# Performance work log

Measured on AMD Instinct MI355X. Metric: run time of the kernel, lower is better.

Reference implementation:

```python
import jax, jax.numpy as jnp
import numpy as np

B, S, C, H, RANK = 8, 1024, 1280, 8, 4
MERGE_SCALE = 1.0   # self.scale
LORA_SCALE = 1.0    # scale arg passed to __call__ (defaults 1.0)


def setup_inputs() -> dict:
    key = jax.random.key(0)
    ks = jax.random.split(key, 20)
    std = 1.0 / np.sqrt(C)
    rstd = 1.0 / np.sqrt(RANK)
    d = {
        "hidden_states": jax.random.normal(ks[0], (B, S, C), jnp.float32),
        "pose_feature": jax.random.normal(ks[1], (B, S, C), jnp.float32),
        # qkv_merge Linear (init to zeros in the module; use small random to exercise the path)
        "qkv_merge_w": jax.random.normal(ks[2], (C, C), jnp.float32) * (0.02 * std),
        "qkv_merge_b": jax.random.normal(ks[3], (C,), jnp.float32) * 0.01,
        # attn.to_q/k/v (bias-free, diffusers default) and to_out[0] (with bias). Stored [in, out].
        "wq": jax.random.normal(ks[4], (C, C), jnp.float32) * std,
        "wk": jax.random.normal(ks[5], (C, C), jnp.float32) * std,
        "wv": jax.random.normal(ks[6], (C, C), jnp.float32) * std,
        "wo": jax.random.normal(ks[7], (C, C), jnp.float32) * std,
        "bo": jax.random.normal(ks[8], (C,), jnp.float32) * 0.01,
        # LoRA layers: down [in, rank], up [rank, out] (up is zeros at init; random here)
        "q_lora_down": jax.random.normal(ks[9], (C, RANK), jnp.float32) * std,
        "q_lora_up": jax.random.normal(ks[10], (RANK, C), jnp.float32) * rstd,
        "k_lora_down": jax.random.normal(ks[11], (C, RANK), jnp.float32) * std,
        "k_lora_up": jax.random.normal(ks[12], (RANK, C), jnp.float32) * rstd,
        "v_lora_down": jax.random.normal(ks[13], (C, RANK), jnp.float32) * std,
        "v_lora_up": jax.random.normal(ks[14], (RANK, C), jnp.float32) * rstd,
        "out_lora_down": jax.random.normal(ks[15], (C, RANK), jnp.float32) * std,
        "out_lora_up": jax.random.normal(ks[16], (RANK, C), jnp.float32) * rstd,
        "num_heads": H,
    }
    return d


def _lora(x, down, up):
    # LoRALinearLayer with network_alpha=None -> scale factor 1
    return (x @ down) @ up


def reference(hidden_states, pose_feature, qkv_merge_w, qkv_merge_b,
              wq, wk, wv, wo, bo,
              q_lora_down, q_lora_up, k_lora_down, k_lora_up,
              v_lora_down, v_lora_up, out_lora_down, out_lora_up,
              num_heads):
    b, s, c = hidden_states.shape
    dh = c // num_heads
    # gated pose-merge (query_condition and key_value_condition -> shared qkv source)
    merged = (hidden_states + pose_feature) @ qkv_merge_w + qkv_merge_b
    x = merged * MERGE_SCALE + hidden_states  # [b, s, c]
    # LoRA-augmented projections
    q = x @ wq + LORA_SCALE * _lora(x, q_lora_down, q_lora_up)
    k = x @ wk + LORA_SCALE * _lora(x, k_lora_down, k_lora_up)
    v = x @ wv + LORA_SCALE * _lora(x, v_lora_down, v_lora_up)
    # head_to_batch_dim -> [b, h, s, dh]
    q = q.reshape(b, s, num_heads, dh).transpose(0, 2, 1, 3)
    k = k.reshape(b, s, num_heads, dh).transpose(0, 2, 1, 3)
    v = v.reshape(b, s, num_heads, dh).transpose(0, 2, 1, 3)
    # attn.get_attention_scores: baddbmm scaled by head_dim**-0.5, then softmax
    scores = jnp.einsum('bhqd,bhkd->bhqk', q, k) * (dh ** -0.5)
    probs = jax.nn.softmax(scores, axis=-1)
    out = jnp.einsum('bhqk,bhkd->bhqd', probs, v)
    # batch_to_head_dim -> [b, s, c]
    out = out.transpose(0, 2, 1, 3).reshape(b, s, c)
    # output projection + LoRA; to_out[1] is dropout (identity at eval)
    out = out @ wo + bo + LORA_SCALE * _lora(out, out_lora_down, out_lora_up)
    # residual_connection=False, rescale_output_factor=1.0
    return out
```

## Files before the change

### kernel.cpp

```cpp
#include <hip/hip_runtime.h>
#include <stdint.h>

typedef unsigned short u16;
typedef __attribute__((ext_vector_type(8))) short short8;
typedef __attribute__((ext_vector_type(4))) float f32x4;

__device__ __forceinline__ float b2f(u16 x){
  union { unsigned u; float f; } v; v.u = ((unsigned)x) << 16; return v.f;
}
__device__ __forceinline__ float b2fs(short x){ return b2f((u16)x); }
__device__ __forceinline__ u16 f2b(float f){
  union { float f; unsigned u; } v; v.f = f;
  unsigned u = v.u;
  u += 0x7FFFu + ((u >> 16) & 1u);
  return (u16)(u >> 16);
}
__device__ __forceinline__ float ldg_f(const void* p, int i, int f32){
  return f32 ? ((const float*)p)[i] : b2f(((const u16*)p)[i]);
}
__device__ __forceinline__ void gld16(const void* g, void* l){
  __builtin_amdgcn_global_load_lds(
      (__attribute__((address_space(1))) void*)(g),
      (__attribute__((address_space(3))) void*)(l), 16, 0, 0);
}
__device__ __forceinline__ unsigned lds_addr(const void* p){
  return (unsigned)(size_t)(__attribute__((address_space(3))) const void*)p;
}
__device__ __forceinline__ short8 ds_r128(unsigned addr){
  short8 r;
  asm volatile("ds_read_b128 %0, %1" : "=v"(r) : "v"(addr));
  return r;
}

__global__ void detect_dtype(const u16* __restrict__ hid, int* __restrict__ flag){
  if (blockIdx.x == 0){
    int lane = threadIdx.x & 63;
    int plaus = 0;
    for (int i = lane; i < 512; i += 64){
      u16 v = hid[2 * i];
      int e = (v >> 7) & 0xFF;
      if ((e >= 100 && e <= 140) || (v & 0x7FFF) == 0) plaus++;
    }
    #pragma unroll
    for (int xm = 1; xm < 64; xm <<= 1) plaus += __shfl_xor(plaus, xm, 64);
    if (threadIdx.x == 0) *flag = (plaus < 400) ? 1 : 0;
  }
}

__global__ void make_t(const void* __restrict__ hid, const void* __restrict__ pose,
                       u16* __restrict__ t, const int* __restrict__ flag){
  int base = (blockIdx.x * 256 + threadIdx.x) * 8;
  short8 o;
  if (*flag){
    #pragma unroll
    for (int j = 0; j < 2; j++){
      float4 a = *(const float4*)((const float*)hid  + base + j * 4);
      float4 b = *(const float4*)((const float*)pose + base + j * 4);
      o[j * 4 + 0] = (short)f2b(a.x + b.x);
      o[j * 4 + 1] = (short)f2b(a.y + b.y);
      o[j * 4 + 2] = (short)f2b(a.z + b.z);
      o[j * 4 + 3] = (short)f2b(a.w + b.w);
    }
  } else {
    short8 a = *(const short8*)((const u16*)hid  + base);
    short8 b = *(const short8*)((const u16*)pose + base);
    #pragma unroll
    for (int j = 0; j < 8; j++) o[j] = (short)f2b(b2fs(a[j]) + b2fs(b[j]));
  }
  *(short8*)(t + base) = o;
}

__global__ void prep_w(const void* __restrict__ w, const void* __restrict__ dn,
                       const void* __restrict__ up, u16* __restrict__ WT,
                       int rowOff, float sc, const int* __restrict__ flag)
{
  __shared__ float tile[64][65];
  const int f = *flag;
  const int k0 = blockIdx.x * 64, n0 = blockIdx.y * 64;
  const int tr  = threadIdx.x >> 2;
  const int tc0 = (threadIdx.x & 3) * 16;
  #pragma unroll
  for (int i = 0; i < 16; i++)
    tile[tr][tc0 + i] = ldg_f(w, (k0 + tr) * 1280 + n0 + tc0 + i, f);
  __syncthreads();
  const int n = n0 + tr;
  float upv[4];
  if (dn){
    #pragma unroll
    for (int r = 0; r < 4; r++) upv[r] = ldg_f(up, r * 1280 + n, f);
  }
  u16 tmp[16];
  #pragma unroll
  for (int i = 0; i < 16; i++){
    int k = k0 + tc0 + i;
    float val = tile[tc0 + i][tr];
    if (dn){
      #pragma unroll
      for (int r = 0; r < 4; r++)
        val += ldg_f(dn, k * 4 + r, f) * upv[r];
    }
    tmp[i] = f2b(val * sc);
  }
  u16* dst = &WT[(rowOff + n) * 1280 + k0 + tc0];
  #pragma unroll
  for (int i = 0; i < 4; i++)
    *(ushort4*)(dst + i * 4) = *(ushort4*)(tmp + i * 4);
}

template<bool BIAS, bool RESID, bool RAWOUT>
__global__ __launch_bounds__(256) void gemm_bt(
    const u16* __restrict__ A, const u16* __restrict__ BT,
    const void* __restrict__ bias, const void* __restrict__ resid,
    void* __restrict__ Cout, int NOUT, int Kdim, const int* __restrict__ flag)
{
  __shared__ alignas(16) u16 As[128 * 32];
  __shared__ alignas(16) u16 Bs[128 * 32];
  const int tid  = threadIdx.x;
  const int lane = tid & 63;
  const int w    = tid >> 6;
  const int wm   = w >> 1, wn = w & 1;
  const int quad = lane >> 4, l15 = lane & 15;
  const int tileM = blockIdx.y << 7;
  const int tileN = blockIdx.x << 7;
  const int f32 = (BIAS || RESID || RAWOUT) ? *flag : 0;

  f32x4 acc[4][4];
  #pragma unroll
  for (int mi = 0; mi < 4; mi++)
    #pragma unroll
    for (int ni = 0; ni < 4; ni++)
      acc[mi][ni] = (f32x4){0.f, 0.f, 0.f, 0.f};

  for (int k0 = 0; k0 < Kdim; k0 += 32){
    {
      int c = tid;
      gld16(&A [(tileM + (c >> 2)) * Kdim + k0 + ((c & 3) << 3)], (char*)As + c * 16);
      gld16(&BT[(tileN + (c >> 2)) * Kdim + k0 + ((c & 3) << 3)], (char*)Bs + c * 16);
      c = tid + 256;
      gld16(&A [(tileM + (c >> 2)) * Kdim + k0 + ((c & 3) << 3)], (char*)As + c * 16);
      gld16(&BT[(tileN + (c >> 2)) * Kdim + k0 + ((c & 3) << 3)], (char*)Bs + c * 16);
    }
    __syncthreads();

    short8 af[4], bfr[4];
    #pragma unroll
    for (int mi = 0; mi < 4; mi++)
      af[mi] = *(const short8*)(As + (wm * 64 + mi * 16 + l15) * 32 + quad * 8);
    #pragma unroll
    for (int ni = 0; ni < 4; ni++)
      bfr[ni] = *(const short8*)(Bs + (wn * 64 + ni * 16 + l15) * 32 + quad * 8);
    #pragma unroll
    for (int mi = 0; mi < 4; mi++)
      #pragma unroll
      for (int ni = 0; ni < 4; ni++)
        acc[mi][ni] = __builtin_amdgcn_mfma_f32_16x16x32_bf16(
            af[mi], bfr[ni], acc[mi][ni], 0, 0, 0);
    __syncthreads();
  }

  #pragma unroll
  for (int mi = 0; mi < 4; mi++){
    #pragma unroll
    for (int ni = 0; ni < 4; ni++){
      int col = tileN + wn * 64 + ni * 16 + l15;
      float bv = 0.f;
      if (BIAS) bv = ldg_f(bias, col, f32);
      #pragma unroll
      for (int r = 0; r < 4; r++){
        int row = tileM + wm * 64 + mi * 16 + quad * 4 + r;
        float v = acc[mi][ni][r] + bv;
        if (RESID) v += ldg_f(resid, row * NOUT + col, f32);
        if (RAWOUT && f32) ((float*)Cout)[row * NOUT + col] = v;
        else               ((u16*)Cout)[row * NOUT + col]   = f2b(v);
      }
    }
  }
}

#define GPHASE(KK, MH)                                                         \
  {                                                                            \
    if ((MH) == 0){                                                            \
      _Pragma("unroll")                                                        \
      for (int n = 0; n < 4; n++){                                             \
        int R = wn * 64 + n * 16 + l15;                                        \
        int sl = (KK) * 4 + quad;                                              \
        bfr[n] = ds_r128(lds_addr(&Bsm[b][R * 64 + ((sl ^ (R & 7)) << 3)]));   \
      }                                                                        \
    }                                                                          \
    short8 af[4];                                                              \
    _Pragma("unroll")                                                          \
    for (int j = 0; j < 4; j++){                                               \
      int R = wm * 128 + ((MH) * 4 + j) * 16 + l15;                            \
      int sl = (KK) * 4 + quad;                                                \
      af[j] = ds_r128(lds_addr(&Asm[b][R * 64 + ((sl ^ (R & 7)) << 3)]));      \
    }                                                                          \
    __builtin_amdgcn_s_barrier();                                              \
    asm volatile("s_waitcnt lgkmcnt(0)" ::: "memory");                         \
    __builtin_amdgcn_sched_barrier(0);                                         \
    __builtin_amdgcn_s_setprio(1);                                             \
    _Pragma("unroll")                                                          \
    for (int j = 0; j < 4; j++)                                                \
      _Pragma("unroll")                                                        \
      for (int n = 0; n < 4; n++)                                              \
        acc[(MH) * 4 + j][n] = __builtin_amdgcn_mfma_f32_16x16x32_bf16(        \
            af[j], bfr[n], acc[(MH) * 4 + j][n], 0, 0, 0);                     \
    __builtin_amdgcn_s_setprio(0);                                             \
    __builtin_amdgcn_s_barrier();                                              \
  }

__global__ __launch_bounds__(512, 2) void gemm256_qkv(
    const u16* __restrict__ A, const u16* __restrict__ BT,
    u16* __restrict__ Cout, u16* __restrict__ vtg,
    int gridX, int Kdim)
{
  __shared__ alignas(16) u16 Asm[2][256 * 64];
  __shared__ alignas(16) u16 Bsm[2][256 * 64];
  const int tid  = threadIdx.x;
  const int lane = tid & 63;
  const int w    = tid >> 6;
  const int wm   = w >> 2, wn = w & 3;
  const int quad = lane >> 4, l15 = lane & 15;

  const int nwg = gridDim.x;
  const int id  = blockIdx.x;
  const int swz = (id & 7) * (nwg >> 3) + (id >> 3);
  const int bx  = swz % gridX;
  const int by  = swz / gridX;
  const int tileM = by << 8;
  const int tileN = bx << 8;

  auto stageHalf = [&](int bufi, int half, int kt){
    const int k0 = kt << 6;
    #pragma unroll
    for (int s = 0; s < 2; s++){
      int cl   = s * 512 + tid;
      int p    = ((half & 1) << 10) + cl;
      int row  = p >> 3;
      int lslt = (p & 7) ^ (row & 7);
      if (half < 2)
        gld16(&A [(tileM + row) * Kdim + k0 + lslt * 8], (char*)Asm[bufi] + p * 16);
      else
        gld16(&BT[(tileN + row) * Kdim + k0 + lslt * 8], (char*)Bsm[bufi] + p * 16);
    }
  };

  f32x4 acc[8][4];
  #pragma unroll
  for (int mi = 0; mi < 8; mi++)
    #pragma unroll
    for (int ni = 0; ni < 4; ni++)
      acc[mi][ni] = (f32x4){0.f, 0.f, 0.f, 0.f};

  const int NT = Kdim >> 6;
  stageHalf(0, 0, 0); stageHalf(0, 1, 0); stageHalf(0, 2, 0); stageHalf(0, 3, 0);
  stageHalf(1, 0, 1); stageHalf(1, 1, 1);
  asm volatile("s_waitcnt vmcnt(4)" ::: "memory");
  __builtin_amdgcn_s_barrier();

  for (int kt = 0; kt < NT; kt++){
    const int b = kt & 1;
    short8 bfr[4];
    if (kt + 1 < NT) stageHalf(b ^ 1, 2, kt + 1);
    GPHASE(0, 0)
    if (kt + 1 < NT) stageHalf(b ^ 1, 3, kt + 1);
    GPHASE(0, 1)
    GPHASE(1, 0)
    GPHASE(1, 1)
    if (kt + 2 < NT){ stageHalf(b, 0, kt + 2); stageHalf(b, 1, kt + 2); }
    if (kt + 1 < NT){
      if (kt + 2 < NT) asm volatile("s_waitcnt vmcnt(4)" ::: "memory");
      else             asm volatile("s_waitcnt vmcnt(0)" ::: "memory");
      __builtin_amdgcn_s_barrier();
    }
  }

  if (tileN >= 2560){
    #pragma unroll
    for (int mi = 0; mi < 8; mi++){
      #pragma unroll
      for (int ni = 0; ni < 4; ni++){
        int col = tileN + wn * 64 + ni * 16 + l15;
        int hd = col - 2560;
        int hh = hd / 160;
        int dd = hd - hh * 160;
        int row0 = tileM + wm * 128 + mi * 16 + quad * 4;
        int bb = row0 >> 10;
        long addr = ((long)((bb * 8 + hh) * 160 + dd) << 10) | (long)(row0 & 1023);
        ushort4 pk;
        pk.x = f2b(acc[mi][ni][0]); pk.y = f2b(acc[mi][ni][1]);
        pk.z = f2b(acc[mi][ni][2]); pk.w = f2b(acc[mi][ni][3]);
        *(ushort4*)&vtg[addr] = pk;
      }
    }
  } else {
    #pragma unroll
    for (int mi = 0; mi < 8; mi++){
      #pragma unroll
      for (int ni = 0; ni < 4; ni++){
        int col = tileN + wn * 64 + ni * 16 + l15;
        #pragma unroll
        for (int r = 0; r < 4; r++){
          int row = tileM + wm * 128 + mi * 16 + quad * 4 + r;
          Cout[row * 2560 + col] = f2b(acc[mi][ni][r]);
        }
      }
    }
  }
}

__global__ __launch_bounds__(256, 2) void attn_mfma(
    const u16* __restrict__ qk, const u16* __restrict__ vtg,
    u16* __restrict__ out)
{
  __shared__ alignas(16) u16 Ks[2 * 64 * 160];
  __shared__ alignas(16) u16 Vt[160 * 64];
  __shared__ alignas(16) u16 Ps[4 * 32 * 72];

  const int tid  = threadIdx.x, lane = tid & 63, wv = tid >> 6;
  const int quad = lane >> 4,   l15  = lane & 15;
  const int bh = ((blockIdx.y >> 3) << 3) | blockIdx.x;
  const int qt = blockIdx.y & 7;
  const int b  = bh >> 3, h = bh & 7;
  const int rowBase = (b << 10) + (qt << 7);
  const int kBase   = b << 10;

  short8 qa[2][5];
  #pragma unroll
  for (int mi = 0; mi < 2; mi++)
    #pragma unroll
    for (int kk = 0; kk < 5; kk++)
      qa[mi][kk] = *(const short8*)&qk[
          (rowBase + wv * 32 + mi * 16 + l15) * 2560 + h * 160 + kk * 32 + quad * 8];

  f32x4 o[2][10];
  #pragma unroll
  for (int mi = 0; mi < 2; mi++)
    #pragma unroll
    for (int ni = 0; ni < 10; ni++)
      o[mi][ni] = (f32x4){0.f, 0.f, 0.f, 0.f};
  float mr[2][4], lr[2][4];
  #pragma unroll
  for (int mi = 0; mi < 2; mi++)
    #pragma unroll
    for (int r = 0; r < 4; r++){ mr[mi][r] = -1e30f; lr[mi][r] = 0.f; }

  #pragma unroll
  for (int i = 0; i < 5; i++){
    int c = tid + (i << 8);
    int kr = c / 20, kc = c % 20;
    gld16(&qk[(kBase + kr) * 2560 + 1280 + h * 160 + (kc << 3)],
          (char*)Ks + c * 16);
  }
  __syncthreads();

  int buf = 0;
  for (int kt = 0; kt < 16; kt++){
    #pragma unroll
    for (int i = 0; i < 5; i++){
      int c = tid + (i << 8);
      int d = c >> 3;
      int l = (c & 7) ^ (d & 7);
      gld16(&vtg[((bh * 160 + d) << 10) + (kt << 6) + (l << 3)],
            (char*)Vt + c * 16);
    }
    if (kt < 15){
      #pragma unroll
      for (int i = 0; i < 5; i++){
        int c = tid + (i << 8);
        int kr = c / 20, kc = c % 20;
        gld16(&qk[(kBase + ((kt + 1) << 6) + kr) * 2560 + 1280 + h * 160 + (kc << 3)],
              (char*)Ks + (buf ^ 1) * 20480 + c * 16);
      }
    }
    const u16* KsR = Ks + buf * 10240;

    f32x4 s[2][4];
    #pragma unroll
    for (int mi = 0; mi < 2; mi++)
      #pragma unroll
      for (int ni = 0; ni < 4; ni++)
        s[mi][ni] = (f32x4){0.f, 0.f, 0.f, 0.f};
    __builtin_amdgcn_s_setprio(1);
    #pragma unroll
    for (int kk = 0; kk < 5; kk++){
      #pragma unroll
      for (int ni = 0; ni < 4; ni++){
        short8 bf = *(const short8*)&KsR[(ni * 16 + l15) * 160 + kk * 32 + quad * 8];
        s[0][ni] = __builtin_amdgcn_mfma_f32_16x16x32_bf16(qa[0][kk], bf, s[0][ni], 0, 0, 0);
        s[1][ni] = __builtin_amdgcn_mfma_f32_16x16x32_bf16(qa[1][kk], bf, s[1][ni], 0, 0, 0);
      }
    }
    __builtin_amdgcn_s_setprio(0);

    float al[2][4];
    #pragma unroll
    for (int mi = 0; mi < 2; mi++){
      #pragma unroll
      for (int r = 0; r < 4; r++){
        float mx = fmaxf(fmaxf(s[mi][0][r], s[mi][1][r]),
                         fmaxf(s[mi][2][r], s[mi][3][r]));
        #pragma unroll
        for (int xm = 1; xm < 16; xm <<= 1) mx = fmaxf(mx, __shfl_xor(mx, xm, 64));
        float mn = fmaxf(mr[mi][r], mx);
        float a  = __expf(mr[mi][r] - mn);
        mr[mi][r] = mn; al[mi][r] = a;
        float sum = 0.f;
        #pragma unroll
        for (int ni = 0; ni < 4; ni++){
          float p = __expf(s[mi][ni][r] - mn);
          s[mi][ni][r] = p; sum += p;
        }
        #pragma unroll
        for (int xm = 1; xm < 16; xm <<= 1) sum += __shfl_xor(sum, xm, 64);
        lr[mi][r] = lr[mi][r] * a + sum;
      }
    }
    #pragma unroll
    for (int mi = 0; mi < 2; mi++)
      #pragma unroll
      for (int ni = 0; ni < 4; ni++)
        #pragma unroll
        for (int r = 0; r < 4; r++)
          Ps[wv * 2304 + (mi * 16 + quad * 4 + r) * 72 + ni * 16 + l15] =
              f2b(s[mi][ni][r]);
    #pragma unroll
    for (int mi = 0; mi < 2; mi++)
      #pragma unroll
      for (int ni = 0; ni < 10; ni++)
        #pragma unroll
        for (int r = 0; r < 4; r++)
          o[mi][ni][r] *= al[mi][r];

    if (kt < 15) asm volatile("s_waitcnt vmcnt(5)" ::: "memory");
    else         asm volatile("s_waitcnt vmcnt(0)" ::: "memory");
    __builtin_amdgcn_s_barrier();

    __builtin_amdgcn_s_setprio(1);
    #pragma unroll
    for (int kk2 = 0; kk2 < 2; kk2++){
      short8 pa0 = *(const short8*)&Ps[wv * 2304 + l15 * 72        + kk2 * 32 + quad * 8];
      short8 pa1 = *(const short8*)&Ps[wv * 2304 + (16 + l15) * 72 + kk2 * 32 + quad * 8];
      #pragma unroll
      for (int ni = 0; ni < 10; ni++){
        short8 vf = *(const short8*)&Vt[((ni * 16 + l15) << 6) +
                                        (((((kk2 << 2) | quad)) ^ (l15 & 7)) << 3)];
        o[0][ni] = __builtin_amdgcn_mfma_f32_16x16x32_bf16(pa0, vf, o[0][ni], 0, 0, 0);
        o[1][ni] = __builtin_amdgcn_mfma_f32_16x16x32_bf16(pa1, vf, o[1][ni], 0, 0, 0);
      }
    }
    __builtin_amdgcn_s_setprio(0);

    asm volatile("s_waitcnt vmcnt(0)" ::: "memory");
    __builtin_amdgcn_s_barrier();
    buf ^= 1;
  }

  #pragma unroll
  for (int mi = 0; mi < 2; mi++){
    #pragma unroll
    for (int r = 0; r < 4; r++){
      float inv = 1.0f / lr[mi][r];
      int row = rowBase + wv * 32 + mi * 16 + quad * 4 + r;
      #pragma unroll
      for (int ni = 0; ni < 10; ni++)
        out[row * 1280 + h * 160 + ni * 16 + l15] = f2b(o[mi][ni][r] * inv);
    }
  }
}

extern "C" void kernel_launch(void* const* d_in, const int* in_sizes, int n_in,
                              void* d_out, int out_size, void* d_ws, size_t ws_size,
                              hipStream_t stream)
{
  const void* hid  = d_in[0];
  const void* pose = d_in[1];
  const void* wm   = d_in[2];
  const void* mb   = d_in[3];
  const void* wq   = d_in[4];
  const void* wk   = d_in[5];
  const void* wv   = d_in[6];
  const void* wo   = d_in[7];
  const void* bo   = d_in[8];
  const void* qd   = d_in[9];
  const void* qu   = d_in[10];
  const void* kd   = d_in[11];
  const void* ku   = d_in[12];
  const void* vd   = d_in[13];
  const void* vu   = d_in[14];
  const void* od   = d_in[15];
  const void* ou   = d_in[16];
  (void)in_sizes; (void)n_in; (void)out_size; (void)ws_size;

  u16* ws   = (u16*)d_ws;
  u16* qk   = ws;
  u16* t    = qk;
  u16* x    = qk + 20971520;
  u16* vtg  = x + 10485760;
  u16* Wbuf = vtg + 10485760;
  u16* attnout = x;
  int* flag = (int*)(Wbuf + 4915200);

  const float qscale = 0.07905694150420949f;

  detect_dtype<<<1, 64, 0, stream>>>((const u16*)hid, flag);
  make_t<<<5120, 256, 0, stream>>>(hid, pose, t, flag);
  prep_w<<<dim3(20, 20), 256, 0, stream>>>(wm, nullptr, nullptr, Wbuf, 0, 1.0f, flag);
  gemm_bt<true, true, false><<<dim3(10, 64), 256, 0, stream>>>(
      t, Wbuf, mb, hid, x, 1280, 1280, flag);
  prep_w<<<dim3(20, 20), 256, 0, stream>>>(wq, qd, qu, Wbuf, 0, qscale, flag);
  prep_w<<<dim3(20, 20), 256, 0, stream>>>(wk, kd, ku, Wbuf, 1280, 1.0f, flag);
  prep_w<<<dim3(20, 20), 256, 0, stream>>>(wv, vd, vu, Wbuf, 2560, 1.0f, flag);
  gemm256_qkv<<<480, 512, 0, stream>>>(x, Wbuf, qk, vtg, 15, 1280);
  attn_mfma<<<dim3(8, 64), 256, 0, stream>>>(qk, vtg, attnout);
  prep_w<<<dim3(20, 20), 256, 0, stream>>>(wo, od, ou, Wbuf, 0, 1.0f, flag);
  gemm_bt<true, false, true><<<dim3(10, 64), 256, 0, stream>>>(
      attnout, Wbuf, bo, nullptr, d_out, 1280, 1280, flag);
}
```

Measured before the change: 509.1 us.

## Software-pipeline LDS fragment reads with MFMA and drop per-phase barriers in QKV GEMM

Restructures the QKV GEMM inner k-loop so LDS fragment reads for the next MFMA group are issued before the current group runs, using partial lgkmcnt waits instead of a full wait. The two barriers around each of the four phases are removed, leaving one barrier per k-tile. This is meant to hide LDS latency behind MFMA work and cut synchronization stalls. It costs more live fragment registers (four A/B buffers), which may push register pressure at 512 threads with two blocks per CU. Both B-half stages are now issued at the start of the iteration.

```diff
diff --git a/kernel.cpp b/kernel.cpp
--- a/kernel.cpp
+++ b/kernel.cpp
@@ -177,36 +177,19 @@
   }
 }
 
-#define GPHASE(KK, MH)                                                         \
-  {                                                                            \
-    if ((MH) == 0){                                                            \
-      _Pragma("unroll")                                                        \
-      for (int n = 0; n < 4; n++){                                             \
-        int R = wn * 64 + n * 16 + l15;                                        \
-        int sl = (KK) * 4 + quad;                                              \
-        bfr[n] = ds_r128(lds_addr(&Bsm[b][R * 64 + ((sl ^ (R & 7)) << 3)]));   \
-      }                                                                        \
-    }                                                                          \
-    short8 af[4];                                                              \
-    _Pragma("unroll")                                                          \
-    for (int j = 0; j < 4; j++){                                               \
-      int R = wm * 128 + ((MH) * 4 + j) * 16 + l15;                            \
-      int sl = (KK) * 4 + quad;                                                \
-      af[j] = ds_r128(lds_addr(&Asm[b][R * 64 + ((sl ^ (R & 7)) << 3)]));      \
-    }                                                                          \
-    __builtin_amdgcn_s_barrier();                                              \
-    asm volatile("s_waitcnt lgkmcnt(0)" ::: "memory");                         \
-    __builtin_amdgcn_sched_barrier(0);                                         \
-    __builtin_amdgcn_s_setprio(1);                                             \
-    _Pragma("unroll")                                                          \
-    for (int j = 0; j < 4; j++)                                                \
-      _Pragma("unroll")                                                        \
-      for (int n = 0; n < 4; n++)                                              \
-        acc[(MH) * 4 + j][n] = __builtin_amdgcn_mfma_f32_16x16x32_bf16(        \
-            af[j], bfr[n], acc[(MH) * 4 + j][n], 0, 0, 0);                     \
-    __builtin_amdgcn_s_setprio(0);                                             \
-    __builtin_amdgcn_s_barrier();                                              \
-  }
+#define LGKM_SB(N)                                                     \
+  asm volatile("s_waitcnt lgkmcnt(" #N ")" ::: "memory");              \
+  __builtin_amdgcn_sched_barrier(0);
+
+#define MFMA16(MH, AF, BF)                                             \
+  __builtin_amdgcn_s_setprio(1);                                       \
+  _Pragma("unroll")                                                    \
+  for (int j = 0; j < 4; j++)                                          \
+    _Pragma("unroll")                                                  \
+    for (int n = 0; n < 4; n++)                                        \
+      acc[(MH) * 4 + j][n] = __builtin_amdgcn_mfma_f32_16x16x32_bf16(  \
+          AF[j], BF[n], acc[(MH) * 4 + j][n], 0, 0, 0);                \
+  __builtin_amdgcn_s_setprio(0);
 
 __global__ __launch_bounds__(512, 2) void gemm256_qkv(
     const u16* __restrict__ A, const u16* __restrict__ BT,
@@ -244,6 +227,23 @@
     }
   };
 
+  auto rdA = [&](short8* dst, int bufi, int mh, int kk){
+    #pragma unroll
+    for (int j = 0; j < 4; j++){
+      int R  = wm * 128 + (mh * 4 + j) * 16 + l15;
+      int sl = kk * 4 + quad;
+      dst[j] = ds_r128(lds_addr(&Asm[bufi][R * 64 + ((sl ^ (R & 7)) << 3)]));
+    }
+  };
+  auto rdB = [&](short8* dst, int bufi, int kk){
+    #pragma unroll
+    for (int n = 0; n < 4; n++){
+      int R  = wn * 64 + n * 16 + l15;
+      int sl = kk * 4 + quad;
+      dst[n] = ds_r128(lds_addr(&Bsm[bufi][R * 64 + ((sl ^ (R & 7)) << 3)]));
+    }
+  };
+
   f32x4 acc[8][4];
   #pragma unroll
   for (int mi = 0; mi < 8; mi++)
@@ -259,13 +259,23 @@
 
   for (int kt = 0; kt < NT; kt++){
     const int b = kt & 1;
-    short8 bfr[4];
-    if (kt + 1 < NT) stageHalf(b ^ 1, 2, kt + 1);
-    GPHASE(0, 0)
-    if (kt + 1 < NT) stageHalf(b ^ 1, 3, kt + 1);
-    GPHASE(0, 1)
-    GPHASE(1, 0)
-    GPHASE(1, 1)
+    if (kt + 1 < NT){ stageHalf(b ^ 1, 2, kt + 1); stageHalf(b ^ 1, 3, kt + 1); }
+
+    short8 aA[4], aB[4], bA[4], bB[4];
+    rdB(bA, b, 0); rdA(aA, b, 0, 0);
+    rdA(aB, b, 1, 0);
+    LGKM_SB(4)
+    MFMA16(0, aA, bA)
+    rdB(bB, b, 1); rdA(aA, b, 0, 1);
+    LGKM_SB(8)
+    MFMA16(1, aB, bA)
+    rdA(aB, b, 1, 1);
+    LGKM_SB(4)
+    MFMA16(0, aA, bB)
+    LGKM_SB(0)
+    MFMA16(1, aB, bB)
+
+    __builtin_amdgcn_s_barrier();
     if (kt + 2 < NT){ stageHalf(b, 0, kt + 2); stageHalf(b, 1, kt + 2); }
     if (kt + 1 < NT){
       if (kt + 2 < NT) asm volatile("s_waitcnt vmcnt(4)" ::: "memory");
```

New measurement: 500.1 us. About the same (-1.8%).
